# Performance work log

Hardware: AMD Instinct MI355X
Metric: run time of the kernel (lower is better)

## Reference

```python
import jax, jax.numpy as jnp
import numpy as np

N_NODES = 100000


def gcn_conv(x, edge_index, W, num_nodes):
    """PyG GCNConv (bias=False): add self-loops, symmetric normalization,
    out[c] = sum_{(r,c) in E'} deg^{-1/2}[r] * deg^{-1/2}[c] * (x @ W)[r]."""
    h = x @ W  # [N, out_dim]
    row, col = edge_index[0], edge_index[1]
    loop = jnp.arange(num_nodes, dtype=row.dtype)
    row = jnp.concatenate([row, loop])
    col = jnp.concatenate([col, loop])
    ones = jnp.ones(row.shape[0], dtype=h.dtype)
    deg = jax.ops.segment_sum(ones, col, num_segments=num_nodes)  # [N]
    dinv = jnp.where(deg > 0, jax.lax.rsqrt(deg), 0.0)
    norm = dinv[row] * dinv[col]  # [E+N]
    msgs = norm[:, None] * h[row]  # gather + scale
    return jax.ops.segment_sum(msgs, col, num_segments=num_nodes)  # scatter-add


def setup_inputs() -> dict:
    key = jax.random.key(0)
    k1, k2, k3, k4 = jax.random.split(key, 4)
    x = jax.random.normal(k1, (N_NODES, 128), dtype=jnp.float32)
    edge_index = jax.random.randint(k2, (2, 3200000), 0, N_NODES, dtype=jnp.int64)
    W1 = jax.random.normal(k3, (128, 32), dtype=jnp.float32) * (1.0 / np.sqrt(128))
    W2 = jax.random.normal(k4, (32, 3), dtype=jnp.float32) * (1.0 / np.sqrt(32))
    return {"x": x, "edge_index": edge_index, "W1": W1, "W2": W2}


def reference(x, edge_index, W1, W2):
    n = x.shape[0]
    hidden1 = jnp.tanh(gcn_conv(x, edge_index, W1, n))  # dropout p=0.0 -> identity
    z = gcn_conv(hidden1, edge_index, W2, n)
    return z  # original returns (z, z, None)
```

## Files before the change

### kernel.cpp

```cpp
#include <hip/hip_runtime.h>
#include <hip/hip_fp16.h>

#define N_NODES 100000
#define N_EDGES 3200000
#define F_IN    128
#define F_HID   32

#define BSHIFT  7
#define BKSZ    128
#define NBKT    ((N_NODES + BKSZ - 1) / BKSZ)
#define CAP     5120
#define CHUNK   4096
#define NBLK_E  ((N_EDGES + CHUNK - 1) / CHUNK)
#define RBITS   17
#define RMASK   0x1FFFF

__device__ __forceinline__ float fast_tanh(float x) {
    float t = __builtin_amdgcn_exp2f(x * 2.88539008f);
    return 1.0f - 2.0f * __builtin_amdgcn_rcpf(t + 1.0f);
}


__global__ __launch_bounds__(512) void k_part(const int* __restrict__ row, const int* __restrict__ col,
                                              int* __restrict__ gcur, unsigned* __restrict__ bkt) {
    __shared__ int hist[NBKT];
    __shared__ int lbase[NBKT];
    __shared__ int gbase[NBKT];
    __shared__ unsigned perm[CHUNK];
    __shared__ unsigned short pb[CHUNK];
    __shared__ int wt[8];
    int t = threadIdx.x;
    for (int i = t; i < NBKT; i += 512) hist[i] = 0;
    __syncthreads();

    int e0 = blockIdx.x * CHUNK;
    int n  = min(CHUNK, N_EDGES - e0);
    int r[8], c[8], rk[8];
#pragma unroll
    for (int k = 0; k < 8; k++) {
        int idx = t + k * 512;
        if (idx < n) {
            r[k]  = row[e0 + idx];
            c[k]  = col[e0 + idx];
            rk[k] = atomicAdd(&hist[c[k] >> BSHIFT], 1);
        }
    }
    __syncthreads();

    {
        int b0 = t * 2;
        int s0 = (b0     < NBKT) ? hist[b0]     : 0;
        int s1 = (b0 + 1 < NBKT) ? hist[b0 + 1] : 0;
        int tsum = s0 + s1;
        int lane = t & 63, wid = t >> 6;
        int incl = tsum;
#pragma unroll
        for (int sh = 1; sh < 64; sh <<= 1) {
            int u = __shfl_up(incl, sh);
            if (lane >= sh) incl += u;
        }
        if (lane == 63) wt[wid] = incl;
        __syncthreads();
        int wpre = 0;
        for (int w = 0; w < wid; w++) wpre += wt[w];
        int excl = wpre + incl - tsum;
        if (b0     < NBKT) lbase[b0]     = excl;
        if (b0 + 1 < NBKT) lbase[b0 + 1] = excl + s0;
    }
    for (int i = t; i < NBKT; i += 512) {
        int h = hist[i];
        gbase[i] = i * CAP + (h ? atomicAdd(&gcur[i], h) : 0);
    }
    __syncthreads();

#pragma unroll
    for (int k = 0; k < 8; k++) {
        int idx = t + k * 512;
        if (idx < n) {
            int b   = c[k] >> BSHIFT;
            int pos = lbase[b] + rk[k];
            perm[pos] = (unsigned)r[k] | ((unsigned)(c[k] & (BKSZ - 1)) << RBITS);
            pb[pos]   = (unsigned short)b;
        }
    }
    __syncthreads();

    for (int i = t; i < n; i += 512) {
        int b = pb[i];
        bkt[gbase[b] + (i - lbase[b])] = perm[i];
    }
}


__global__ __launch_bounds__(1024) void k_bucket(unsigned* __restrict__ bkt,
                                                 const int* __restrict__ gcur,
                                                 int* __restrict__ off, int* __restrict__ end,
                                                 float* __restrict__ dinv) {
    __shared__ unsigned stg[CAP];
    __shared__ int cnt[BKSZ];
    __shared__ int cur[BKSZ];
    __shared__ int wtot[2];
    int t = threadIdx.x, b = blockIdx.x;
    int s = b * CAP, m = gcur[b];
    if (t < BKSZ) cnt[t] = 0;
    __syncthreads();
    for (int i = t; i < m; i += 1024) {
        unsigned x = bkt[s + i];
        stg[i] = x;
        atomicAdd(&cnt[x >> RBITS], 1);
    }
    __syncthreads();

    int lane = t & 63, wid = t >> 6;
    int v = 0, v4 = 0, incl = 0;
    if (t < BKSZ) {
        v  = cnt[t];
        v4 = (v + 3) & ~3;
        incl = v4;
        #pragma unroll
        for (int sh = 1; sh < 64; sh <<= 1) {
            int u = __shfl_up(incl, sh);
            if (lane >= sh) incl += u;
        }
        if (lane == 63) wtot[wid] = incl;
    }
    __syncthreads();
    if (t < BKSZ) {
        int wpre = (wid == 1) ? wtot[0] : 0;
        int excl = wpre + incl - v4;
        int base = s + excl;
        cur[t] = base;
        int g = b * BKSZ + t;
        if (g < N_NODES) {
            off[g]  = base;
            end[g]  = base + v4;
            dinv[g] = rsqrtf((float)(v + 1));
        }
        for (int j = v; j < v4; j++) bkt[base + j] = N_NODES;
    }
    __syncthreads();
    for (int i = t; i < m; i += 1024) {
        unsigned x = stg[i];
        int p = atomicAdd(&cur[x >> RBITS], 1);
        bkt[p] = x & RMASK;
    }
}


__global__ __launch_bounds__(256) void k_gemm1(const float* __restrict__ x, const float* __restrict__ W1,
                                               const float* __restrict__ dinv, unsigned* __restrict__ h1s) {
    __shared__ float Wlds[F_IN * F_HID];
    int t = threadIdx.x;
    for (int i = t; i < F_IN * F_HID; i += 256) Wlds[i] = W1[i];
    __syncthreads();

    int gid = blockIdx.x * 256 + t;
    int r = gid >> 3, f4 = gid & 7;
    if (r > N_NODES) return;
    if (r == N_NODES) {
        ((uint2*)h1s)[(size_t)r * 8 + f4] = make_uint2(0u, 0u);
        return;
    }

    const float4* x4  = (const float4*)(x + (size_t)r * F_IN);
    const float4* Wl4 = (const float4*)Wlds;
    float ax = 0.f, ay = 0.f, az = 0.f, aw = 0.f;
#pragma unroll
    for (int k4 = 0; k4 < F_IN / 4; k4++) {
        float4 xv = x4[k4];
        float4 w0 = Wl4[(4 * k4 + 0) * 8 + f4];
        ax += xv.x * w0.x; ay += xv.x * w0.y; az += xv.x * w0.z; aw += xv.x * w0.w;
        float4 w1 = Wl4[(4 * k4 + 1) * 8 + f4];
        ax += xv.y * w1.x; ay += xv.y * w1.y; az += xv.y * w1.z; aw += xv.y * w1.w;
        float4 w2 = Wl4[(4 * k4 + 2) * 8 + f4];
        ax += xv.z * w2.x; ay += xv.z * w2.y; az += xv.z * w2.z; aw += xv.z * w2.w;
        float4 w3 = Wl4[(4 * k4 + 3) * 8 + f4];
        ax += xv.w * w3.x; ay += xv.w * w3.y; az += xv.w * w3.z; aw += xv.w * w3.w;
    }
    float di = dinv[r];
    unsigned p01 = (unsigned)__half_as_ushort(__float2half(di * ax))
                 | ((unsigned)__half_as_ushort(__float2half(di * ay)) << 16);
    unsigned p23 = (unsigned)__half_as_ushort(__float2half(di * az))
                 | ((unsigned)__half_as_ushort(__float2half(di * aw)) << 16);
    ((uint2*)h1s)[(size_t)r * 8 + f4] = make_uint2(p01, p23);
}


__global__ __launch_bounds__(256) void k_conv1(const int* __restrict__ off, const int* __restrict__ end,
                                               const int* __restrict__ srt, const float* __restrict__ dinv,
                                               const unsigned* __restrict__ h1s,
                                               const float* __restrict__ W2, float* __restrict__ h2s4) {
    int t = threadIdx.x;
    if (blockIdx.x == 0 && t < 4) h2s4[(size_t)N_NODES * 4 + t] = 0.0f;
    int lane = t & 63, wid = t >> 6;
    int q = lane >> 3, o = lane & 7;
    int c = (blockIdx.x * 4 + wid) * 8 + q;

    int b = off[c], ep = end[c];
    const char* h1b = (const char*)h1s;
    unsigned oo = (unsigned)(o << 3);
    uint2 sv = *(const uint2*)(h1b + (((unsigned)c << 6) + oo));

    float a0a = 0.f, a1a = 0.f, a2a = 0.f, a3a = 0.f;
    float a0b = 0.f, a1b = 0.f, a2b = 0.f, a3b = 0.f;
    float a0c = 0.f, a1c = 0.f, a2c = 0.f, a3c = 0.f;
    float a0d = 0.f, a1d = 0.f, a2d = 0.f, a3d = 0.f;

    int p = b;
    while (__any(p < ep)) {
        int r0 = N_NODES, r1 = N_NODES, r2 = N_NODES, r3 = N_NODES;
        if (p < ep) {
            int4 rs = *(const int4*)(srt + p);
            r0 = rs.x; r1 = rs.y; r2 = rs.z; r3 = rs.w;
        }
        uint2 v0 = *(const uint2*)(h1b + (((unsigned)r0 << 6) + oo));
        uint2 v1 = *(const uint2*)(h1b + (((unsigned)r1 << 6) + oo));
        uint2 v2 = *(const uint2*)(h1b + (((unsigned)r2 << 6) + oo));
        uint2 v3 = *(const uint2*)(h1b + (((unsigned)r3 << 6) + oo));
        a0a += __low2float(*(const __half2*)&v0.x);  a1a += __high2float(*(const __half2*)&v0.x);
        a2a += __low2float(*(const __half2*)&v0.y);  a3a += __high2float(*(const __half2*)&v0.y);
        a0b += __low2float(*(const __half2*)&v1.x);  a1b += __high2float(*(const __half2*)&v1.x);
        a2b += __low2float(*(const __half2*)&v1.y);  a3b += __high2float(*(const __half2*)&v1.y);
        a0c += __low2float(*(const __half2*)&v2.x);  a1c += __high2float(*(const __half2*)&v2.x);
        a2c += __low2float(*(const __half2*)&v2.y);  a3c += __high2float(*(const __half2*)&v2.y);
        a0d += __low2float(*(const __half2*)&v3.x);  a1d += __high2float(*(const __half2*)&v3.x);
        a2d += __low2float(*(const __half2*)&v3.y);  a3d += __high2float(*(const __half2*)&v3.y);
        p += 4;
    }

    float di = dinv[c];
    float f0 = (a0a + a0b) + (a0c + a0d) + __low2float(*(const __half2*)&sv.x);
    float f1 = (a1a + a1b) + (a1c + a1d) + __high2float(*(const __half2*)&sv.x);
    float f2 = (a2a + a2b) + (a2c + a2d) + __low2float(*(const __half2*)&sv.y);
    float f3 = (a3a + a3b) + (a3c + a3d) + __high2float(*(const __half2*)&sv.y);

    float h0 = fast_tanh(di * f0);
    float h1 = fast_tanh(di * f1);
    float h2 = fast_tanh(di * f2);
    float h3 = fast_tanh(di * f3);

    const float* Wp = W2 + (o << 2) * 3;
    float p0 = h0 * Wp[0] + h1 * Wp[3] + h2 * Wp[6] + h3 * Wp[9];
    float p1 = h0 * Wp[1] + h1 * Wp[4] + h2 * Wp[7] + h3 * Wp[10];
    float p2 = h0 * Wp[2] + h1 * Wp[5] + h2 * Wp[8] + h3 * Wp[11];
#pragma unroll
    for (int m = 1; m <= 4; m <<= 1) {
        p0 += __shfl_xor(p0, m);
        p1 += __shfl_xor(p1, m);
        p2 += __shfl_xor(p2, m);
    }
    if (o < 4) {
        float vv = (o == 0) ? p0 : (o == 1) ? p1 : (o == 2) ? p2 : 0.0f;
        h2s4[(size_t)c * 4 + o] = (o < 3) ? di * vv : 0.0f;
    }
}


__global__ __launch_bounds__(256) void k_conv2(const int* __restrict__ off, const int* __restrict__ end,
                                               const int* __restrict__ srt, const float* __restrict__ dinv,
                                               const float* __restrict__ h2s4, float* __restrict__ out) {
    int gt = blockIdx.x * 256 + threadIdx.x;
    int c = gt >> 2, j = gt & 3;
    if (c >= N_NODES) return;

    const float4* h2v = (const float4*)h2s4;
    int b = off[c], ep = end[c];
    float4 sv = h2v[c];
    float ax = (j == 0) ? sv.x : 0.0f;
    float ay = (j == 0) ? sv.y : 0.0f;
    float az = (j == 0) ? sv.z : 0.0f;

    for (int p = b + 4 * j; p < ep; p += 16) {
        int4 rs = *(const int4*)(srt + p);
        float4 v0 = h2v[rs.x];
        float4 v1 = h2v[rs.y];
        float4 v2 = h2v[rs.z];
        float4 v3 = h2v[rs.w];
        ax += (v0.x + v1.x) + (v2.x + v3.x);
        ay += (v0.y + v1.y) + (v2.y + v3.y);
        az += (v0.z + v1.z) + (v2.z + v3.z);
    }
#pragma unroll
    for (int m = 1; m <= 2; m <<= 1) {
        ax += __shfl_xor(ax, m);
        ay += __shfl_xor(ay, m);
        az += __shfl_xor(az, m);
    }

    float di = dinv[c];
    if (j < 3) {
        float a = (j == 0) ? ax : (j == 1) ? ay : az;
        out[(size_t)c * 3 + j] = di * a;
    }
}


extern "C" void kernel_launch(void* const* d_in, const int* in_sizes, int n_in,
                              void* d_out, int out_size, void* d_ws, size_t ws_size,
                              hipStream_t stream) {
    const float* x   = (const float*)d_in[0];
    const int*   ei  = (const int*)d_in[1];
    const float* W1  = (const float*)d_in[2];
    const float* W2  = (const float*)d_in[3];
    float*       out = (float*)d_out;

    const int* row = ei;
    const int* col = ei + N_EDGES;

    char* ws = (char*)d_ws;
    unsigned* bkt = (unsigned*)ws;
    int*      srt = (int*)ws;
    char*     p   = ws + 4ull * NBKT * CAP;
    int*      gcur = (int*)p;                 p += 4ull * ((NBKT + 63) & ~63);
    int*      off  = (int*)p;                 p += 4ull * N_NODES;
    int*      end  = (int*)p;                 p += 4ull * N_NODES;
    float*    dinv = (float*)p;               p += 4ull * N_NODES;
    unsigned* h1s  = (unsigned*)p;            p += 64ull * (N_NODES + 1);
    float*    h2s4 = (float*)p;

    const int B = 256;
    hipMemsetAsync(gcur, 0, 4ull * NBKT, stream);
    hipLaunchKernelGGL(k_part,   dim3(NBLK_E), dim3(512),  0, stream, row, col, gcur, bkt);
    hipLaunchKernelGGL(k_bucket, dim3(NBKT),   dim3(1024), 0, stream, bkt, gcur, off, end, dinv);
    hipLaunchKernelGGL(k_gemm1,  dim3(((N_NODES + 1) * 8 + B - 1) / B), dim3(B), 0, stream, x, W1, dinv, h1s);
    hipLaunchKernelGGL(k_conv1,  dim3(N_NODES / 32), dim3(B), 0, stream,
                       off, end, srt, dinv, h1s, W2, h2s4);
    hipLaunchKernelGGL(k_conv2,  dim3((4 * N_NODES + B - 1) / B), dim3(B), 0, stream,
                       off, end, srt, dinv, h2s4, out);
}
```

Before: 228.2 us.

## Split hidden features into two halves and aggregate in two passes

Stores the fp16 hidden features as two separate 16-feature arrays of 32 bytes per node instead of one 64-byte row, and splits the first aggregation into two kernels, each gathering one half. Each pass's gather working set is half the size (about 3.2 MB), so it is more likely to stay resident in cache during the random neighbour gathers. The cost is reading the sorted edge list twice, an extra partial-sum buffer written and read back, and one more kernel launch.

New measurement: 246.9 us. 1.08x slower.

```diff
diff --git a/kernel.cpp b/kernel.cpp
--- a/kernel.cpp
+++ b/kernel.cpp
@@ -14,6 +14,7 @@
 #define NBLK_E  ((N_EDGES + CHUNK - 1) / CHUNK)
 #define RBITS   17
 #define RMASK   0x1FFFF
+#define NBLK1   ((N_NODES + 63) / 64)
 
 __device__ __forceinline__ float fast_tanh(float x) {
     float t = __builtin_amdgcn_exp2f(x * 2.88539008f);
@@ -148,7 +149,8 @@
 
 
 __global__ __launch_bounds__(256) void k_gemm1(const float* __restrict__ x, const float* __restrict__ W1,
-                                               const float* __restrict__ dinv, unsigned* __restrict__ h1s) {
+                                               const float* __restrict__ dinv,
+                                               unsigned* __restrict__ h1a, unsigned* __restrict__ h1b) {
     __shared__ float Wlds[F_IN * F_HID];
     int t = threadIdx.x;
     for (int i = t; i < F_IN * F_HID; i += 256) Wlds[i] = W1[i];
@@ -158,7 +160,8 @@
     int r = gid >> 3, f4 = gid & 7;
     if (r > N_NODES) return;
     if (r == N_NODES) {
-        ((uint2*)h1s)[(size_t)r * 8 + f4] = make_uint2(0u, 0u);
+        if (f4 < 4) ((uint2*)h1a)[(size_t)r * 4 + f4]       = make_uint2(0u, 0u);
+        else        ((uint2*)h1b)[(size_t)r * 4 + (f4 - 4)] = make_uint2(0u, 0u);
         return;
     }
 
@@ -182,24 +185,26 @@
                  | ((unsigned)__half_as_ushort(__float2half(di * ay)) << 16);
     unsigned p23 = (unsigned)__half_as_ushort(__float2half(di * az))
                  | ((unsigned)__half_as_ushort(__float2half(di * aw)) << 16);
-    ((uint2*)h1s)[(size_t)r * 8 + f4] = make_uint2(p01, p23);
-}
-
-
-__global__ __launch_bounds__(256) void k_conv1(const int* __restrict__ off, const int* __restrict__ end,
-                                               const int* __restrict__ srt, const float* __restrict__ dinv,
-                                               const unsigned* __restrict__ h1s,
-                                               const float* __restrict__ W2, float* __restrict__ h2s4) {
+    if (f4 < 4) ((uint2*)h1a)[(size_t)r * 4 + f4]       = make_uint2(p01, p23);
+    else        ((uint2*)h1b)[(size_t)r * 4 + (f4 - 4)] = make_uint2(p01, p23);
+}
+
+
+__global__ __launch_bounds__(256) void k_conv1a(const int* __restrict__ off, const int* __restrict__ end,
+                                                const int* __restrict__ srt,
+                                                const unsigned* __restrict__ h1a,
+                                                float* __restrict__ part) {
     int t = threadIdx.x;
-    if (blockIdx.x == 0 && t < 4) h2s4[(size_t)N_NODES * 4 + t] = 0.0f;
     int lane = t & 63, wid = t >> 6;
-    int q = lane >> 3, o = lane & 7;
-    int c = (blockIdx.x * 4 + wid) * 8 + q;
-
-    int b = off[c], ep = end[c];
-    const char* h1b = (const char*)h1s;
+    int q = lane >> 2, o = lane & 3;
+    int c = (blockIdx.x * 4 + wid) * 16 + q;
+    int cs = (c < N_NODES) ? c : N_NODES;
+    int b = 0, ep = 0;
+    if (c < N_NODES) { b = off[c]; ep = end[c]; }
+
+    const char* hb = (const char*)h1a;
     unsigned oo = (unsigned)(o << 3);
-    uint2 sv = *(const uint2*)(h1b + (((unsigned)c << 6) + oo));
+    uint2 sv = *(const uint2*)(hb + (((unsigned)cs << 5) + oo));
 
     float a0a = 0.f, a1a = 0.f, a2a = 0.f, a3a = 0.f;
     float a0b = 0.f, a1b = 0.f, a2b = 0.f, a3b = 0.f;
@@ -213,10 +218,10 @@
             int4 rs = *(const int4*)(srt + p);
             r0 = rs.x; r1 = rs.y; r2 = rs.z; r3 = rs.w;
         }
-        uint2 v0 = *(const uint2*)(h1b + (((unsigned)r0 << 6) + oo));
-        uint2 v1 = *(const uint2*)(h1b + (((unsigned)r1 << 6) + oo));
-        uint2 v2 = *(const uint2*)(h1b + (((unsigned)r2 << 6) + oo));
-        uint2 v3 = *(const uint2*)(h1b + (((unsigned)r3 << 6) + oo));
+        uint2 v0 = *(const uint2*)(hb + (((unsigned)r0 << 5) + oo));
+        uint2 v1 = *(const uint2*)(hb + (((unsigned)r1 << 5) + oo));
+        uint2 v2 = *(const uint2*)(hb + (((unsigned)r2 << 5) + oo));
+        uint2 v3 = *(const uint2*)(hb + (((unsigned)r3 << 5) + oo));
         a0a += __low2float(*(const __half2*)&v0.x);  a1a += __high2float(*(const __half2*)&v0.x);
         a2a += __low2float(*(const __half2*)&v0.y);  a3a += __high2float(*(const __half2*)&v0.y);
         a0b += __low2float(*(const __half2*)&v1.x);  a1b += __high2float(*(const __half2*)&v1.x);
@@ -228,31 +233,90 @@
         p += 4;
     }
 
-    float di = dinv[c];
     float f0 = (a0a + a0b) + (a0c + a0d) + __low2float(*(const __half2*)&sv.x);
     float f1 = (a1a + a1b) + (a1c + a1d) + __high2float(*(const __half2*)&sv.x);
     float f2 = (a2a + a2b) + (a2c + a2d) + __low2float(*(const __half2*)&sv.y);
     float f3 = (a3a + a3b) + (a3c + a3d) + __high2float(*(const __half2*)&sv.y);
 
-    float h0 = fast_tanh(di * f0);
-    float h1 = fast_tanh(di * f1);
-    float h2 = fast_tanh(di * f2);
-    float h3 = fast_tanh(di * f3);
-
-    const float* Wp = W2 + (o << 2) * 3;
-    float p0 = h0 * Wp[0] + h1 * Wp[3] + h2 * Wp[6] + h3 * Wp[9];
-    float p1 = h0 * Wp[1] + h1 * Wp[4] + h2 * Wp[7] + h3 * Wp[10];
-    float p2 = h0 * Wp[2] + h1 * Wp[5] + h2 * Wp[8] + h3 * Wp[11];
-#pragma unroll
-    for (int m = 1; m <= 4; m <<= 1) {
+    if (c < N_NODES)
+        *(float4*)(part + ((size_t)c << 4) + (o << 2)) = make_float4(f0, f1, f2, f3);
+}
+
+
+__global__ __launch_bounds__(256) void k_conv1b(const int* __restrict__ off, const int* __restrict__ end,
+                                                const int* __restrict__ srt, const float* __restrict__ dinv,
+                                                const unsigned* __restrict__ h1b,
+                                                const float* __restrict__ part,
+                                                const float* __restrict__ W2, float* __restrict__ h2s4) {
+    int t = threadIdx.x;
+    if (blockIdx.x == 0 && t < 4) h2s4[(size_t)N_NODES * 4 + t] = 0.0f;
+    int lane = t & 63, wid = t >> 6;
+    int q = lane >> 2, o = lane & 3;
+    int c = (blockIdx.x * 4 + wid) * 16 + q;
+    int cs = (c < N_NODES) ? c : N_NODES;
+    int b = 0, ep = 0;
+    if (c < N_NODES) { b = off[c]; ep = end[c]; }
+
+    const char* hb = (const char*)h1b;
+    unsigned oo = (unsigned)(o << 3);
+    uint2 sv = *(const uint2*)(hb + (((unsigned)cs << 5) + oo));
+
+    float a0a = 0.f, a1a = 0.f, a2a = 0.f, a3a = 0.f;
+    float a0b = 0.f, a1b = 0.f, a2b = 0.f, a3b = 0.f;
+    float a0c = 0.f, a1c = 0.f, a2c = 0.f, a3c = 0.f;
+    float a0d = 0.f, a1d = 0.f, a2d = 0.f, a3d = 0.f;
+
+    int p = b;
+    while (__any(p < ep)) {
+        int r0 = N_NODES, r1 = N_NODES, r2 = N_NODES, r3 = N_NODES;
+        if (p < ep) {
+            int4 rs = *(const int4*)(srt + p);
+            r0 = rs.x; r1 = rs.y; r2 = rs.z; r3 = rs.w;
+        }
+        uint2 v0 = *(const uint2*)(hb + (((unsigned)r0 << 5) + oo));
+        uint2 v1 = *(const uint2*)(hb + (((unsigned)r1 << 5) + oo));
+        uint2 v2 = *(const uint2*)(hb + (((unsigned)r2 << 5) + oo));
+        uint2 v3 = *(const uint2*)(hb + (((unsigned)r3 << 5) + oo));
+        a0a += __low2float(*(const __half2*)&v0.x);  a1a += __high2float(*(const __half2*)&v0.x);
+        a2a += __low2float(*(const __half2*)&v0.y);  a3a += __high2float(*(const __half2*)&v0.y);
+        a0b += __low2float(*(const __half2*)&v1.x);  a1b += __high2float(*(const __half2*)&v1.x);
+        a2b += __low2float(*(const __half2*)&v1.y);  a3b += __high2float(*(const __half2*)&v1.y);
+        a0c += __low2float(*(const __half2*)&v2.x);  a1c += __high2float(*(const __half2*)&v2.x);
+        a2c += __low2float(*(const __half2*)&v2.y);  a3c += __high2float(*(const __half2*)&v2.y);
+        a0d += __low2float(*(const __half2*)&v3.x);  a1d += __high2float(*(const __half2*)&v3.x);
+        a2d += __low2float(*(const __half2*)&v3.y);  a3d += __high2float(*(const __half2*)&v3.y);
+        p += 4;
+    }
+    if (c >= N_NODES) return;
+
+    float f0 = (a0a + a0b) + (a0c + a0d) + __low2float(*(const __half2*)&sv.x);
+    float f1 = (a1a + a1b) + (a1c + a1d) + __high2float(*(const __half2*)&sv.x);
+    float f2 = (a2a + a2b) + (a2c + a2d) + __low2float(*(const __half2*)&sv.y);
+    float f3 = (a3a + a3b) + (a3c + a3d) + __high2float(*(const __half2*)&sv.y);
+
+    float4 pa = *(const float4*)(part + ((size_t)c << 4) + (o << 2));
+    float di = dinv[c];
+    float hA0 = fast_tanh(di * pa.x), hA1 = fast_tanh(di * pa.y);
+    float hA2 = fast_tanh(di * pa.z), hA3 = fast_tanh(di * pa.w);
+    float hB0 = fast_tanh(di * f0),   hB1 = fast_tanh(di * f1);
+    float hB2 = fast_tanh(di * f2),   hB3 = fast_tanh(di * f3);
+
+    const float* WA = W2 + (o << 2) * 3;
+    const float* WB = W2 + (16 + (o << 2)) * 3;
+    float p0 = hA0 * WA[0] + hA1 * WA[3] + hA2 * WA[6] + hA3 * WA[9]
+             + hB0 * WB[0] + hB1 * WB[3] + hB2 * WB[6] + hB3 * WB[9];
+    float p1 = hA0 * WA[1] + hA1 * WA[4] + hA2 * WA[7] + hA3 * WA[10]
+             + hB0 * WB[1] + hB1 * WB[4] + hB2 * WB[7] + hB3 * WB[10];
+    float p2 = hA0 * WA[2] + hA1 * WA[5] + hA2 * WA[8] + hA3 * WA[11]
+             + hB0 * WB[2] + hB1 * WB[5] + hB2 * WB[8] + hB3 * WB[11];
+#pragma unroll
+    for (int m = 1; m <= 2; m <<= 1) {
         p0 += __shfl_xor(p0, m);
         p1 += __shfl_xor(p1, m);
         p2 += __shfl_xor(p2, m);
     }
-    if (o < 4) {
-        float vv = (o == 0) ? p0 : (o == 1) ? p1 : (o == 2) ? p2 : 0.0f;
-        h2s4[(size_t)c * 4 + o] = (o < 3) ? di * vv : 0.0f;
-    }
+    float vv = (o == 0) ? p0 : (o == 1) ? p1 : (o == 2) ? p2 : 0.0f;
+    h2s4[(size_t)c * 4 + o] = (o < 3) ? di * vv : 0.0f;
 }
 
 
@@ -315,16 +379,20 @@
     int*      off  = (int*)p;                 p += 4ull * N_NODES;
     int*      end  = (int*)p;                 p += 4ull * N_NODES;
     float*    dinv = (float*)p;               p += 4ull * N_NODES;
-    unsigned* h1s  = (unsigned*)p;            p += 64ull * (N_NODES + 1);
+    unsigned* h1a  = (unsigned*)p;            p += 32ull * (N_NODES + 2);
+    unsigned* h1b  = (unsigned*)p;            p += 32ull * (N_NODES + 2);
+    float*    part = (float*)p;               p += 64ull * N_NODES;
     float*    h2s4 = (float*)p;
 
     const int B = 256;
     hipMemsetAsync(gcur, 0, 4ull * NBKT, stream);
     hipLaunchKernelGGL(k_part,   dim3(NBLK_E), dim3(512),  0, stream, row, col, gcur, bkt);
     hipLaunchKernelGGL(k_bucket, dim3(NBKT),   dim3(1024), 0, stream, bkt, gcur, off, end, dinv);
-    hipLaunchKernelGGL(k_gemm1,  dim3(((N_NODES + 1) * 8 + B - 1) / B), dim3(B), 0, stream, x, W1, dinv, h1s);
-    hipLaunchKernelGGL(k_conv1,  dim3(N_NODES / 32), dim3(B), 0, stream,
-                       off, end, srt, dinv, h1s, W2, h2s4);
+    hipLaunchKernelGGL(k_gemm1,  dim3(((N_NODES + 1) * 8 + B - 1) / B), dim3(B), 0, stream,
+                       x, W1, dinv, h1a, h1b);
+    hipLaunchKernelGGL(k_conv1a, dim3(NBLK1), dim3(B), 0, stream, off, end, srt, h1a, part);
+    hipLaunchKernelGGL(k_conv1b, dim3(NBLK1), dim3(B), 0, stream,
+                       off, end, srt, dinv, h1b, part, W2, h2s4);
     hipLaunchKernelGGL(k_conv2,  dim3((4 * N_NODES + B - 1) / B), dim3(B), 0, stream,
                        off, end, srt, dinv, h2s4, out);
 }
```

## Compute first-layer GEMM with fp16 MFMA on 16-row tiles

Applied to the files above, without the earlier changes.

Replaces the scalar FP32 dot-product GEMM for x@W1 with a matrix-core path. Each wavefront converts a 16x128 tile of x to fp16 in LDS and issues mfma_f32_16x16x32_f16 against an fp16, transposed and padded copy of W1. The goal is to cut ALU and LDS-read cost in the dense projection. In exchange the inputs are rounded to fp16 before the multiply, which may add some precision loss, and the output is written with scattered 2-byte stores.

Measured after the change: 215.4 us. 5.6% less time.

```diff
diff --git a/kernel.cpp b/kernel.cpp
--- a/kernel.cpp
+++ b/kernel.cpp
@@ -14,6 +14,11 @@
 #define NBLK_E  ((N_EDGES + CHUNK - 1) / CHUNK)
 #define RBITS   17
 #define RMASK   0x1FFFF
+
+typedef _Float16 f16;
+typedef f16   f16x8 __attribute__((ext_vector_type(8)));
+typedef float f32x4 __attribute__((ext_vector_type(4)));
+#define WPAD 136
 
 __device__ __forceinline__ float fast_tanh(float x) {
     float t = __builtin_amdgcn_exp2f(x * 2.88539008f);
@@ -149,40 +154,59 @@
 
 __global__ __launch_bounds__(256) void k_gemm1(const float* __restrict__ x, const float* __restrict__ W1,
                                                const float* __restrict__ dinv, unsigned* __restrict__ h1s) {
-    __shared__ float Wlds[F_IN * F_HID];
+    __shared__ f16 WH[F_HID * WPAD];
+    __shared__ f16 XH[4][16 * WPAD];
     int t = threadIdx.x;
-    for (int i = t; i < F_IN * F_HID; i += 256) Wlds[i] = W1[i];
-    __syncthreads();
-
-    int gid = blockIdx.x * 256 + t;
-    int r = gid >> 3, f4 = gid & 7;
-    if (r > N_NODES) return;
-    if (r == N_NODES) {
-        ((uint2*)h1s)[(size_t)r * 8 + f4] = make_uint2(0u, 0u);
-        return;
-    }
-
-    const float4* x4  = (const float4*)(x + (size_t)r * F_IN);
-    const float4* Wl4 = (const float4*)Wlds;
-    float ax = 0.f, ay = 0.f, az = 0.f, aw = 0.f;
-#pragma unroll
-    for (int k4 = 0; k4 < F_IN / 4; k4++) {
-        float4 xv = x4[k4];
-        float4 w0 = Wl4[(4 * k4 + 0) * 8 + f4];
-        ax += xv.x * w0.x; ay += xv.x * w0.y; az += xv.x * w0.z; aw += xv.x * w0.w;
-        float4 w1 = Wl4[(4 * k4 + 1) * 8 + f4];
-        ax += xv.y * w1.x; ay += xv.y * w1.y; az += xv.y * w1.z; aw += xv.y * w1.w;
-        float4 w2 = Wl4[(4 * k4 + 2) * 8 + f4];
-        ax += xv.z * w2.x; ay += xv.z * w2.y; az += xv.z * w2.z; aw += xv.z * w2.w;
-        float4 w3 = Wl4[(4 * k4 + 3) * 8 + f4];
-        ax += xv.w * w3.x; ay += xv.w * w3.y; az += xv.w * w3.z; aw += xv.w * w3.w;
-    }
-    float di = dinv[r];
-    unsigned p01 = (unsigned)__half_as_ushort(__float2half(di * ax))
-                 | ((unsigned)__half_as_ushort(__float2half(di * ay)) << 16);
-    unsigned p23 = (unsigned)__half_as_ushort(__float2half(di * az))
-                 | ((unsigned)__half_as_ushort(__float2half(di * aw)) << 16);
-    ((uint2*)h1s)[(size_t)r * 8 + f4] = make_uint2(p01, p23);
+    for (int i = t; i < F_IN * F_HID; i += 256) {
+        int k = i >> 5, f = i & 31;
+        WH[f * WPAD + k] = (f16)W1[i];
+    }
+    if (blockIdx.x == 0 && t < 8)
+        ((uint2*)h1s)[(size_t)N_NODES * 8 + t] = make_uint2(0u, 0u);
+    __syncthreads();
+
+    int l = t & 63, w = t >> 6;
+    int tile = blockIdx.x * 4 + w;
+    if (tile >= N_NODES / 16) return;
+    int R0 = tile * 16;
+
+    {
+        int row = l >> 2, seg = l & 3;
+        const float4* xg = (const float4*)(x + (size_t)(R0 + row) * F_IN) + seg * 8;
+        f16* dst = &XH[w][row * WPAD + seg * 32];
+#pragma unroll
+        for (int j = 0; j < 4; j++) {
+            float4 a = xg[2 * j], b = xg[2 * j + 1];
+            f16x8 v;
+            v[0] = (f16)a.x; v[1] = (f16)a.y; v[2] = (f16)a.z; v[3] = (f16)a.w;
+            v[4] = (f16)b.x; v[5] = (f16)b.y; v[6] = (f16)b.z; v[7] = (f16)b.w;
+            *(f16x8*)(dst + j * 8) = v;
+        }
+    }
+
+    f32x4 acc0 = {0.f, 0.f, 0.f, 0.f};
+    f32x4 acc1 = {0.f, 0.f, 0.f, 0.f};
+    int lo = l & 15, hi = l >> 4;
+    const f16* arow  = &XH[w][lo * WPAD + hi * 8];
+    const f16* b0row = &WH[lo * WPAD + hi * 8];
+    const f16* b1row = &WH[(16 + lo) * WPAD + hi * 8];
+#pragma unroll
+    for (int s = 0; s < 4; s++) {
+        f16x8 af  = *(const f16x8*)(arow  + s * 32);
+        f16x8 bf0 = *(const f16x8*)(b0row + s * 32);
+        f16x8 bf1 = *(const f16x8*)(b1row + s * 32);
+        acc0 = __builtin_amdgcn_mfma_f32_16x16x32_f16(af, bf0, acc0, 0, 0, 0);
+        acc1 = __builtin_amdgcn_mfma_f32_16x16x32_f16(af, bf1, acc1, 0, 0, 0);
+    }
+
+    _Float16* h1h = (_Float16*)h1s;
+    int rbase = R0 + hi * 4;
+#pragma unroll
+    for (int i = 0; i < 4; i++) {
+        float d = dinv[rbase + i];
+        h1h[(size_t)(rbase + i) * 32 + lo]      = (f16)(d * acc0[i]);
+        h1h[(size_t)(rbase + i) * 32 + 16 + lo] = (f16)(d * acc1[i]);
+    }
 }
 
 
@@ -319,10 +343,11 @@
     float*    h2s4 = (float*)p;
 
     const int B = 256;
+    const int NTILE = N_NODES / 16;
     hipMemsetAsync(gcur, 0, 4ull * NBKT, stream);
     hipLaunchKernelGGL(k_part,   dim3(NBLK_E), dim3(512),  0, stream, row, col, gcur, bkt);
     hipLaunchKernelGGL(k_bucket, dim3(NBKT),   dim3(1024), 0, stream, bkt, gcur, off, end, dinv);
-    hipLaunchKernelGGL(k_gemm1,  dim3(((N_NODES + 1) * 8 + B - 1) / B), dim3(B), 0, stream, x, W1, dinv, h1s);
+    hipLaunchKernelGGL(k_gemm1,  dim3((NTILE + 3) / 4), dim3(B), 0, stream, x, W1, dinv, h1s);
     hipLaunchKernelGGL(k_conv1,  dim3(N_NODES / 32), dim3(B), 0, stream,
                        off, end, srt, dinv, h1s, W2, h2s4);
     hipLaunchKernelGGL(k_conv2,  dim3((4 * N_NODES + B - 1) / B), dim3(B), 0, stream,
```
